# Kernel tuning notes

Measured on AMD Instinct MI355X. Metric: run time of the kernel, lower is better.

## Reference

```python
import jax, jax.numpy as jnp
import numpy as np

N_HEADS = 16
D_K = 64
DIM = 1024
NEG = -1e12
LN_EPS = 1e-5


def setup_inputs() -> dict:
    key = jax.random.key(0)
    ks = jax.random.split(key, 8)
    B, S, D = 2, 2048, DIM
    H, K = N_HEADS, D_K
    f = lambda k, shp: jax.random.normal(k, shp, dtype=jnp.float32)
    scale = 0.02
    return {
        "input_Q": f(ks[0], (B, S, D)),
        "input_K": f(ks[1], (B, S, D)),
        "input_V": f(ks[2], (B, S, D)),
        "attention_mask": jax.random.randint(ks[3], (B, S), 0, 2, dtype=jnp.int32),
        "W_Q": f(ks[4], (H * K, D)) * scale,  # nn.Linear weight layout [out, in]
        "W_K": f(ks[5], (H * K, D)) * scale,
        "W_V": f(ks[6], (H * K, D)) * scale,
        "W_O": f(ks[7], (D, H * K)) * scale,
        "gamma": jnp.ones((D,), jnp.float32),
        "beta": jnp.zeros((D,), jnp.float32),
    }


def reference(input_Q, input_K, input_V, attention_mask, W_Q, W_K, W_V, W_O, gamma, beta):
    B, S, D = input_Q.shape

    def proj(x, W):  # [B,S,D] @ [HK,D]^T -> [B,H,S,K]
        return (x @ W.T).reshape(B, S, N_HEADS, D_K).transpose(0, 2, 1, 3)

    Q = proj(input_Q, W_Q)
    K = proj(input_K, W_K)
    V = proj(input_V, W_V)

    scores = jnp.einsum('bhqk,bhsk->bhqs', Q, K) / np.float32(np.sqrt(D_K))

    # Faithful reproduction of scores_mask (including its inverted-looking logic):
    # mask = clamp(padding_mask + strict_upper_tri - 1, min=0); scores += (1-mask)*NEG
    am = attention_mask.astype(scores.dtype)[:, None, None, :]          # [B,1,1,S]
    low_tri = jnp.triu(jnp.ones((S, S), scores.dtype), k=1)             # 1 - tril(ones)
    m = jnp.maximum(am + low_tri - 1.0, 0.0)
    scores = scores + (1.0 - m) * NEG

    attn = jax.nn.softmax(scores, axis=-1)
    ctx = jnp.einsum('bhqs,bhsk->bhqk', attn, V)                        # [B,H,S,K]
    ctx = ctx.transpose(0, 2, 1, 3).reshape(B, S, N_HEADS * D_K)

    out = ctx @ W_O.T + input_Q                                         # fc + residual
    mu = jnp.mean(out, axis=-1, keepdims=True)
    var = jnp.var(out, axis=-1, keepdims=True)
    return (out - mu) / jnp.sqrt(var + LN_EPS) * gamma + beta
```

## Files before the change

kernel.cpp:

```cpp
#include <hip/hip_runtime.h>

#define NH    16
#define DK    64
#define DIM   1024
#define BATCH 2
#define SEQ   2048
#define MROWS (BATCH*SEQ)
#define BK    64
#define QSCALE 0.18033688011112043f
#define SENT   -44.0f
#define PCONST 5.684341886080802e-14f

typedef unsigned short bfraw;
typedef __attribute__((ext_vector_type(8))) __bf16 bf16x8;
typedef __attribute__((ext_vector_type(8))) unsigned short u16x8;
typedef __attribute__((ext_vector_type(4))) float f32x4;

__device__ __forceinline__ float bf2f(bfraw u) {
    union { unsigned int i; float f; } x; x.i = ((unsigned int)u) << 16; return x.f;
}
__device__ __forceinline__ bfraw f2bf(float f) {
    union { float f; unsigned int i; } x; x.f = f;
    unsigned int r = x.i + 0x7FFFu + ((x.i >> 16) & 1u);
    return (bfraw)(r >> 16);
}
__device__ __forceinline__ bfraw f2bf_trunc(float f) {
    union { float f; unsigned int i; } x; x.f = f;
    return (bfraw)(x.i >> 16);
}
__device__ __forceinline__ float fexp2(float x) {
#if __has_builtin(__builtin_amdgcn_exp2f)
    return __builtin_amdgcn_exp2f(x);
#else
    return exp2f(x);
#endif
}

__device__ __forceinline__ void gload16(const bfraw* g, bfraw* l) {
#if __has_builtin(__builtin_amdgcn_global_load_lds)
    __builtin_amdgcn_global_load_lds(
        (const __attribute__((address_space(1))) unsigned int*)g,
        (__attribute__((address_space(3))) unsigned int*)l, 16, 0, 0);
#else
    *(u16x8*)(l + (threadIdx.x & 63) * 8) = *(const u16x8*)g;
#endif
}

__device__ __forceinline__ float block_reduce(float val, float* rbuf, int op) {
    const int lane = threadIdx.x & 63, wave = threadIdx.x >> 6;
    #pragma unroll
    for (int off = 32; off; off >>= 1) {
        float o = __shfl_xor(val, off, 64);
        val = op ? (val + o) : fmaxf(val, o);
    }
    if (lane == 0) rbuf[wave] = val;
    __syncthreads();
    float r = op ? (rbuf[0] + rbuf[1] + rbuf[2] + rbuf[3])
                 : fmaxf(fmaxf(rbuf[0], rbuf[1]), fmaxf(rbuf[2], rbuf[3]));
    __syncthreads();
    return r;
}

__global__ __launch_bounds__(256) void cvt_kernel(
        const float* __restrict__ x0, const float* __restrict__ x1, const float* __restrict__ x2,
        const float* __restrict__ w0, const float* __restrict__ w1, const float* __restrict__ w2,
        const float* __restrict__ w3, bfraw* __restrict__ Xb, bfraw* __restrict__ Wb) {
    const int t = blockIdx.y;
    const float* src; bfraw* dst; int n;
    if (t < 3) { src = (t == 0) ? x0 : (t == 1) ? x1 : x2; dst = Xb + t * (MROWS * DIM); n = MROWS * DIM; }
    else { int u = t - 3; src = (u == 0) ? w0 : (u == 1) ? w1 : (u == 2) ? w2 : w3;
           dst = Wb + u * (DIM * DIM); n = DIM * DIM; }
    int idx = (blockIdx.x * 256 + threadIdx.x) * 8;
    if (idx >= n) return;
    f32x4 a = *(const f32x4*)(src + idx);
    f32x4 b = *(const f32x4*)(src + idx + 4);
    u16x8 o;
    #pragma unroll
    for (int j = 0; j < 4; j++) { o[j] = f2bf(a[j]); o[4 + j] = f2bf(b[j]); }
    *(u16x8*)(dst + idx) = o;
}

__device__ __forceinline__ void gemm128(const bfraw* __restrict__ A, const bfraw* __restrict__ B,
                                        int m0, int n0, f32x4 acc[4][4]) {
    __shared__ __align__(16) bfraw As[128 * BK];
    __shared__ __align__(16) bfraw Bs[128 * BK];
    const int tid = threadIdx.x, wave = tid >> 6;
    const int lane = tid & 63, lrow = lane & 15, quad = lane >> 4;
    const int wy = wave >> 1, wx = wave & 1;
    const int swz = lrow & 7;
    const int srow = tid >> 3;
    const int schunk = ((tid & 7) ^ (srow & 7)) << 3;
    const bfraw* ga[4]; const bfraw* gb[4];
    #pragma unroll
    for (int g = 0; g < 4; g++) {
        ga[g] = A + (m0 + g * 32 + srow) * DIM + schunk;
        gb[g] = B + (n0 + g * 32 + srow) * DIM + schunk;
    }
    bfraw* la = As + wave * 512;
    bfraw* lb = Bs + wave * 512;

    #pragma unroll
    for (int i = 0; i < 4; i++)
        #pragma unroll
        for (int j = 0; j < 4; j++) { f32x4 z = {0.f, 0.f, 0.f, 0.f}; acc[i][j] = z; }

    for (int k0 = 0; k0 < DIM; k0 += BK) {
        __syncthreads();
        #pragma unroll
        for (int g = 0; g < 4; g++) gload16(ga[g] + k0, la + g * 2048);
        #pragma unroll
        for (int g = 0; g < 4; g++) gload16(gb[g] + k0, lb + g * 2048);
        __syncthreads();
        #pragma unroll
        for (int ks = 0; ks < 2; ks++) {
            const int c = (ks << 2) | quad;
            bf16x8 af[4], bfg[4];
            #pragma unroll
            for (int mi = 0; mi < 4; mi++)
                af[mi] = *(const bf16x8*)&As[(wy * 64 + mi * 16 + lrow) * BK + ((c ^ swz) << 3)];
            #pragma unroll
            for (int ni = 0; ni < 4; ni++)
                bfg[ni] = *(const bf16x8*)&Bs[(wx * 64 + ni * 16 + lrow) * BK + ((c ^ swz) << 3)];
            #pragma unroll
            for (int mi = 0; mi < 4; mi++)
                #pragma unroll
                for (int ni = 0; ni < 4; ni++)
                    acc[mi][ni] = __builtin_amdgcn_mfma_f32_16x16x32_bf16(af[mi], bfg[ni], acc[mi][ni], 0, 0, 0);
        }
    }
}

__global__ __launch_bounds__(256) void qkv_gemm(
        const bfraw* __restrict__ Xb, const bfraw* __restrict__ Wb,
        bfraw* __restrict__ Qp, bfraw* __restrict__ Kp, bfraw* __restrict__ Vt) {
    const int which = blockIdx.z;
    const bfraw* A = Xb + which * (MROWS * DIM);
    const bfraw* B = Wb + which * (DIM * DIM);
    bfraw* O = (which == 0) ? Qp : (which == 1) ? Kp : Vt;
    const int m0 = blockIdx.x * 128, n0 = blockIdx.y * 128;
    f32x4 acc[4][4];
    gemm128(A, B, m0, n0, acc);
    const int lane = threadIdx.x & 63, wave = threadIdx.x >> 6;
    const int lrow = lane & 15, quad = lane >> 4;
    const int wy = wave >> 1, wx = wave & 1;
    const float scale = (which == 0) ? QSCALE : 1.0f;
    #pragma unroll
    for (int mi = 0; mi < 4; mi++)
        #pragma unroll
        for (int ni = 0; ni < 4; ni++)
            #pragma unroll
            for (int i = 0; i < 4; i++) {
                int m = m0 + wy * 64 + mi * 16 + quad * 4 + i;
                int n = n0 + wx * 64 + ni * 16 + lrow;
                int b = m >> 11, s = m & (SEQ - 1), h = n >> 6, kk = n & (DK - 1);
                bfraw v = f2bf(acc[mi][ni][i] * scale);
                if (which == 2) O[(((b * NH + h) * DK) + kk) * SEQ + s] = v;
                else            O[(((b * NH + h) * SEQ) + s) * DK + kk] = v;
            }
}

__global__ __launch_bounds__(256) void vsum_kernel(const bfraw* __restrict__ Vt,
                                                   float* __restrict__ Scum) {
    __shared__ float Ts[32][65];
    const int bh = blockIdx.x, tid = threadIdx.x;
    const int d = tid & 63, part = tid >> 6;
    const bfraw* vrow = Vt + (bh * DK + d) * SEQ;
    for (int qt = part * 8; qt < part * 8 + 8; qt++) {
        float s = 0.f;
        #pragma unroll
        for (int j = 0; j < 64; j += 8) {
            u16x8 v = *(const u16x8*)(vrow + qt * 64 + j);
            #pragma unroll
            for (int e = 0; e < 8; e++) s += bf2f(v[e]);
        }
        Ts[qt][d] = s;
    }
    __syncthreads();
    if (tid < 64) {
        float run = 0.f;
        for (int qt = 0; qt < 32; qt++) {
            Scum[(bh * 32 + qt) * 64 + tid] = run;
            run += Ts[qt][tid];
        }
    }
}

__global__ __launch_bounds__(256) void attn_flash(
        const bfraw* __restrict__ Qp, const bfraw* __restrict__ Kp, const bfraw* __restrict__ Vt,
        const float* __restrict__ Scum, const int* __restrict__ mask, bfraw* __restrict__ Ctx) {
    __shared__ __align__(16) bfraw Ks[64 * 72];
    __shared__ __align__(16) bfraw Vs[64 * 72];
    __shared__ __align__(16) bfraw Pw[4][16 * 68];
    __shared__ unsigned short Mk[SEQ];
    const int bh = blockIdx.x, qt = blockIdx.y;
    const int b = bh >> 4, h = bh & 15;
    const int tid = threadIdx.x, wave = tid >> 6, lane = tid & 63;
    const int lrow = lane & 15, quad = lane >> 4;
    const int baseK = ((b * NH + h) * SEQ) * DK;
    const int baseV = ((b * NH + h) * DK) * SEQ;
    const int qbase = qt * 64 + wave * 16;
    const int ldr = tid >> 2, ldc = (tid & 3) << 4;
    const int diagKt = qt * 64;

    for (int i = tid; i < SEQ; i += 256) Mk[i] = (unsigned short)(mask[b * SEQ + i] != 0);

    bf16x8 qf[2];
    qf[0] = *(const bf16x8*)(Qp + baseK + (qbase + lrow) * DK + quad * 8);
    qf[1] = *(const bf16x8*)(Qp + baseK + (qbase + lrow) * DK + 32 + quad * 8);

    f32x4 O[4]; float lsum[4];
    #pragma unroll
    for (int n = 0; n < 4; n++) {
        float base = PCONST * Scum[(bh * 32 + qt) * 64 + n * 16 + lrow];
        #pragma unroll
        for (int i = 0; i < 4; i++) O[n][i] = base;
    }
    #pragma unroll
    for (int i = 0; i < 4; i++) lsum[i] = 0.f;

    __syncthreads();

    for (int kt0 = diagKt; kt0 < SEQ; kt0 += 64) {
        u16x8 k0 = *(const u16x8*)(Kp + baseK + (kt0 + ldr) * DK + ldc);
        u16x8 k1 = *(const u16x8*)(Kp + baseK + (kt0 + ldr) * DK + ldc + 8);
        u16x8 v0 = *(const u16x8*)(Vt + baseV + ldr * SEQ + kt0 + ldc);
        u16x8 v1 = *(const u16x8*)(Vt + baseV + ldr * SEQ + kt0 + ldc + 8);
        __syncthreads();
        *(u16x8*)&Ks[ldr * 72 + ldc]     = k0;
        *(u16x8*)&Ks[ldr * 72 + ldc + 8] = k1;
        *(u16x8*)&Vs[ldr * 72 + ldc]     = v0;
        *(u16x8*)&Vs[ldr * 72 + ldc + 8] = v1;
        __syncthreads();

        f32x4 S[4];
        #pragma unroll
        for (int n = 0; n < 4; n++) {
            f32x4 z = {0.f, 0.f, 0.f, 0.f}; S[n] = z;
            #pragma unroll
            for (int ks = 0; ks < 2; ks++) {
                bf16x8 kb = *(const bf16x8*)&Ks[(n * 16 + lrow) * 72 + ks * 32 + quad * 8];
                S[n] = __builtin_amdgcn_mfma_f32_16x16x32_bf16(qf[ks], kb, S[n], 0, 0, 0);
            }
        }

        float p[4][4];
        if (kt0 == diagKt) {
            #pragma unroll
            for (int n = 0; n < 4; n++) {
                int s = kt0 + n * 16 + lrow;
                bool mk = (Mk[s] != 0);
                #pragma unroll
                for (int i = 0; i < 4; i++) {
                    bool valid = mk && (s > qbase + quad * 4 + i);
                    p[n][i] = fexp2(valid ? S[n][i] : SENT);
                }
            }
        } else {
            #pragma unroll
            for (int n = 0; n < 4; n++) {
                bool mk = (Mk[kt0 + n * 16 + lrow] != 0);
                #pragma unroll
                for (int i = 0; i < 4; i++) p[n][i] = fexp2(mk ? S[n][i] : SENT);
            }
        }

        #pragma unroll
        for (int i = 0; i < 4; i++) lsum[i] += (p[0][i] + p[1][i]) + (p[2][i] + p[3][i]);

        #pragma unroll
        for (int n = 0; n < 4; n++)
            #pragma unroll
            for (int i = 0; i < 4; i++)
                Pw[wave][(quad * 4 + i) * 68 + n * 16 + lrow] = f2bf_trunc(p[n][i]);

        bf16x8 pa0 = *(const bf16x8*)&Pw[wave][lrow * 68 + quad * 8];
        bf16x8 pa1 = *(const bf16x8*)&Pw[wave][lrow * 68 + 32 + quad * 8];
        #pragma unroll
        for (int n = 0; n < 4; n++)
            #pragma unroll
            for (int ks = 0; ks < 2; ks++) {
                bf16x8 vb = *(const bf16x8*)&Vs[(n * 16 + lrow) * 72 + ks * 32 + quad * 8];
                O[n] = __builtin_amdgcn_mfma_f32_16x16x32_bf16(ks ? pa1 : pa0, vb, O[n], 0, 0, 0);
            }
    }

    float inv[4];
    #pragma unroll
    for (int i = 0; i < 4; i++) {
        float r = lsum[i];
        #pragma unroll
        for (int off = 1; off < 16; off <<= 1) r += __shfl_xor(r, off, 64);
        inv[i] = 1.0f / (r + (float)diagKt * PCONST);
    }
    #pragma unroll
    for (int n = 0; n < 4; n++)
        #pragma unroll
        for (int i = 0; i < 4; i++)
            Ctx[(b * SEQ + qbase + quad * 4 + i) * DIM + h * DK + n * 16 + lrow] = f2bf(O[n][i] * inv[i]);
}

__global__ __launch_bounds__(256) void out_gemm(
        const bfraw* __restrict__ Ctx, const bfraw* __restrict__ WoB, float* __restrict__ C) {
    const int m0 = blockIdx.x * 128, n0 = blockIdx.y * 128;
    f32x4 acc[4][4];
    gemm128(Ctx, WoB, m0, n0, acc);
    const int lane = threadIdx.x & 63, wave = threadIdx.x >> 6;
    const int lrow = lane & 15, quad = lane >> 4;
    const int wy = wave >> 1, wx = wave & 1;
    #pragma unroll
    for (int mi = 0; mi < 4; mi++)
        #pragma unroll
        for (int ni = 0; ni < 4; ni++)
            #pragma unroll
            for (int i = 0; i < 4; i++) {
                int m = m0 + wy * 64 + mi * 16 + quad * 4 + i;
                int n = n0 + wx * 64 + ni * 16 + lrow;
                C[m * DIM + n] = acc[mi][ni][i];
            }
}

__global__ __launch_bounds__(256) void ln_kernel(
        const float* __restrict__ C, const float* __restrict__ Xq,
        const float* __restrict__ gamma, const float* __restrict__ beta,
        float* __restrict__ out) {
    __shared__ float rbuf[4];
    const int m = blockIdx.x, tid = threadIdx.x;
    const float* crow = C + m * DIM;
    const float* xrow = Xq + m * DIM;
    float v[4]; float s = 0.f, s2 = 0.f;
    #pragma unroll
    for (int i = 0; i < 4; i++) {
        int d = tid + (i << 8);
        float x = crow[d] + xrow[d];
        v[i] = x; s += x; s2 += x * x;
    }
    float S  = block_reduce(s,  rbuf, 1);
    float S2 = block_reduce(s2, rbuf, 1);
    float mu  = S * (1.0f / DIM);
    float var = S2 * (1.0f / DIM) - mu * mu;
    float rstd = rsqrtf(var + 1e-5f);
    #pragma unroll
    for (int i = 0; i < 4; i++) {
        int d = tid + (i << 8);
        out[m * DIM + d] = (v[i] - mu) * rstd * gamma[d] + beta[d];
    }
}

extern "C" void kernel_launch(void* const* d_in, const int* in_sizes, int n_in,
                              void* d_out, int out_size, void* d_ws, size_t ws_size,
                              hipStream_t stream) {
    const float* Xq    = (const float*)d_in[0];
    const float* Xk    = (const float*)d_in[1];
    const float* Xv    = (const float*)d_in[2];
    const int*   mask  = (const int*)  d_in[3];
    const float* Wq    = (const float*)d_in[4];
    const float* Wk    = (const float*)d_in[5];
    const float* Wv    = (const float*)d_in[6];
    const float* Wo    = (const float*)d_in[7];
    const float* gamma = (const float*)d_in[8];
    const float* beta  = (const float*)d_in[9];
    float* out = (float*)d_out;

    char* ws = (char*)d_ws;
    bfraw* Xb   = (bfraw*)(ws);
    bfraw* Wb   = (bfraw*)(ws + (24u << 20));
    bfraw* Qp   = (bfraw*)(ws + (32u << 20));
    bfraw* Kp   = (bfraw*)(ws + (40u << 20));
    bfraw* Vt   = (bfraw*)(ws + (48u << 20));
    bfraw* Ctx  = (bfraw*)(ws + (56u << 20));
    float* C    = (float*)(ws);
    float* Scum = (float*)(ws + (16u << 20));

    dim3 blk(256);
    cvt_kernel<<<dim3(MROWS * DIM / (256 * 8), 7), blk, 0, stream>>>(Xq, Xk, Xv, Wq, Wk, Wv, Wo, Xb, Wb);
    qkv_gemm  <<<dim3(MROWS / 128, DIM / 128, 3),  blk, 0, stream>>>(Xb, Wb, Qp, Kp, Vt);
    vsum_kernel<<<dim3(BATCH * NH),                blk, 0, stream>>>(Vt, Scum);
    attn_flash<<<dim3(BATCH * NH, SEQ / 64),       blk, 0, stream>>>(Qp, Kp, Vt, Scum, mask, Ctx);
    out_gemm  <<<dim3(MROWS / 128, DIM / 128),     blk, 0, stream>>>(Ctx, Wb + 3 * (DIM * DIM), C);
    ln_kernel <<<dim3(MROWS),                      blk, 0, stream>>>(C, Xq, gamma, beta, out);
}
```

Before: 243.3 us.

## Widen attention query tile to 128 rows with swizzled direct-to-LDS K/V loads

Result: slower. 264.3 us (+8.6%).

```diff
diff --git a/kernel.cpp b/kernel.cpp
--- a/kernel.cpp
+++ b/kernel.cpp
@@ -188,115 +188,135 @@
 __global__ __launch_bounds__(256) void attn_flash(
         const bfraw* __restrict__ Qp, const bfraw* __restrict__ Kp, const bfraw* __restrict__ Vt,
         const float* __restrict__ Scum, const int* __restrict__ mask, bfraw* __restrict__ Ctx) {
-    __shared__ __align__(16) bfraw Ks[64 * 72];
-    __shared__ __align__(16) bfraw Vs[64 * 72];
-    __shared__ __align__(16) bfraw Pw[4][16 * 68];
+    __shared__ __align__(16) bfraw Ks[64 * 64];
+    __shared__ __align__(16) bfraw Vs[64 * 64];
+    __shared__ __align__(16) bfraw Pw[4][32 * 68];
     __shared__ unsigned short Mk[SEQ];
-    const int bh = blockIdx.x, qt = blockIdx.y;
+    const int bh = blockIdx.x, yy = blockIdx.y;
+    const int qt = (yy & 1) ? (15 - (yy >> 1)) : (yy >> 1);
     const int b = bh >> 4, h = bh & 15;
     const int tid = threadIdx.x, wave = tid >> 6, lane = tid & 63;
     const int lrow = lane & 15, quad = lane >> 4;
     const int baseK = ((b * NH + h) * SEQ) * DK;
     const int baseV = ((b * NH + h) * DK) * SEQ;
-    const int qbase = qt * 64 + wave * 16;
-    const int ldr = tid >> 2, ldc = (tid & 3) << 4;
-    const int diagKt = qt * 64;
+    const int blockDiag = qt * 128;
+    const int qbase = blockDiag + wave * 32;
+    const int tW = qt * 2 + (wave >> 1);
+    const int wstart = blockDiag + (wave >> 1) * 64;
+    const int srow8 = lane >> 3;
+    const int gchunk = ((lane & 7) ^ srow8) << 3;
 
     for (int i = tid; i < SEQ; i += 256) Mk[i] = (unsigned short)(mask[b * SEQ + i] != 0);
 
-    bf16x8 qf[2];
-    qf[0] = *(const bf16x8*)(Qp + baseK + (qbase + lrow) * DK + quad * 8);
-    qf[1] = *(const bf16x8*)(Qp + baseK + (qbase + lrow) * DK + 32 + quad * 8);
-
-    f32x4 O[4]; float lsum[4];
+    bf16x8 qf[2][2];
+    #pragma unroll
+    for (int set = 0; set < 2; set++)
+        #pragma unroll
+        for (int ks = 0; ks < 2; ks++)
+            qf[set][ks] = *(const bf16x8*)(Qp + baseK + (qbase + set * 16 + lrow) * DK + ks * 32 + quad * 8);
+
+    f32x4 Oa[2][4]; float lsum[2][4];
     #pragma unroll
     for (int n = 0; n < 4; n++) {
-        float base = PCONST * Scum[(bh * 32 + qt) * 64 + n * 16 + lrow];
-        #pragma unroll
-        for (int i = 0; i < 4; i++) O[n][i] = base;
-    }
-    #pragma unroll
-    for (int i = 0; i < 4; i++) lsum[i] = 0.f;
-
-    __syncthreads();
-
-    for (int kt0 = diagKt; kt0 < SEQ; kt0 += 64) {
-        u16x8 k0 = *(const u16x8*)(Kp + baseK + (kt0 + ldr) * DK + ldc);
-        u16x8 k1 = *(const u16x8*)(Kp + baseK + (kt0 + ldr) * DK + ldc + 8);
-        u16x8 v0 = *(const u16x8*)(Vt + baseV + ldr * SEQ + kt0 + ldc);
-        u16x8 v1 = *(const u16x8*)(Vt + baseV + ldr * SEQ + kt0 + ldc + 8);
+        float base = PCONST * Scum[(bh * 32 + tW) * 64 + n * 16 + lrow];
+        #pragma unroll
+        for (int set = 0; set < 2; set++) {
+            #pragma unroll
+            for (int i = 0; i < 4; i++) Oa[set][n][i] = base;
+        }
+    }
+    #pragma unroll
+    for (int set = 0; set < 2; set++)
+        #pragma unroll
+        for (int i = 0; i < 4; i++) lsum[set][i] = 0.f;
+
+    for (int kt0 = blockDiag; kt0 < SEQ; kt0 += 64) {
         __syncthreads();
-        *(u16x8*)&Ks[ldr * 72 + ldc]     = k0;
-        *(u16x8*)&Ks[ldr * 72 + ldc + 8] = k1;
-        *(u16x8*)&Vs[ldr * 72 + ldc]     = v0;
-        *(u16x8*)&Vs[ldr * 72 + ldc + 8] = v1;
+        #pragma unroll
+        for (int r = 0; r < 2; r++) {
+            const int row0 = r * 32 + wave * 8;
+            gload16(Kp + baseK + (kt0 + row0 + srow8) * DK + gchunk, Ks + row0 * 64);
+            gload16(Vt + baseV + (row0 + srow8) * SEQ + kt0 + gchunk, Vs + row0 * 64);
+        }
         __syncthreads();
 
-        f32x4 S[4];
-        #pragma unroll
-        for (int n = 0; n < 4; n++) {
-            f32x4 z = {0.f, 0.f, 0.f, 0.f}; S[n] = z;
-            #pragma unroll
-            for (int ks = 0; ks < 2; ks++) {
-                bf16x8 kb = *(const bf16x8*)&Ks[(n * 16 + lrow) * 72 + ks * 32 + quad * 8];
-                S[n] = __builtin_amdgcn_mfma_f32_16x16x32_bf16(qf[ks], kb, S[n], 0, 0, 0);
+        if (kt0 >= wstart) {
+            bf16x8 kf[2][4];
+            #pragma unroll
+            for (int n = 0; n < 4; n++) {
+                const int s = n * 16 + lrow;
+                #pragma unroll
+                for (int ks = 0; ks < 2; ks++)
+                    kf[ks][n] = *(const bf16x8*)&Ks[s * 64 + ((((ks << 2) | quad) ^ (s & 7)) << 3)];
             }
-        }
-
-        float p[4][4];
-        if (kt0 == diagKt) {
-            #pragma unroll
-            for (int n = 0; n < 4; n++) {
-                int s = kt0 + n * 16 + lrow;
-                bool mk = (Mk[s] != 0);
-                #pragma unroll
-                for (int i = 0; i < 4; i++) {
-                    bool valid = mk && (s > qbase + quad * 4 + i);
-                    p[n][i] = fexp2(valid ? S[n][i] : SENT);
+            f32x4 S[2][4];
+            #pragma unroll
+            for (int set = 0; set < 2; set++)
+                #pragma unroll
+                for (int n = 0; n < 4; n++) {
+                    f32x4 z = {0.f, 0.f, 0.f, 0.f};
+                    z = __builtin_amdgcn_mfma_f32_16x16x32_bf16(qf[set][0], kf[0][n], z, 0, 0, 0);
+                    S[set][n] = __builtin_amdgcn_mfma_f32_16x16x32_bf16(qf[set][1], kf[1][n], S[set][n] = z, 0, 0, 0);
+                }
+
+            const bool diagzone = (kt0 < blockDiag + 128);
+            #pragma unroll
+            for (int set = 0; set < 2; set++) {
+                #pragma unroll
+                for (int n = 0; n < 4; n++) {
+                    const int s = kt0 + n * 16 + lrow;
+                    const bool mk = (Mk[s] != 0);
+                    #pragma unroll
+                    for (int i = 0; i < 4; i++) {
+                        bool valid = diagzone ? (mk && (s > qbase + set * 16 + quad * 4 + i)) : mk;
+                        float p = fexp2(valid ? S[set][n][i] : SENT);
+                        lsum[set][i] += p;
+                        Pw[wave][(set * 16 + quad * 4 + i) * 68 + n * 16 + lrow] = f2bf_trunc(p);
+                    }
                 }
             }
-        } else {
+
+            bf16x8 vf[2][4];
             #pragma unroll
             for (int n = 0; n < 4; n++) {
-                bool mk = (Mk[kt0 + n * 16 + lrow] != 0);
-                #pragma unroll
-                for (int i = 0; i < 4; i++) p[n][i] = fexp2(mk ? S[n][i] : SENT);
+                const int d = n * 16 + lrow;
+                #pragma unroll
+                for (int ks = 0; ks < 2; ks++)
+                    vf[ks][n] = *(const bf16x8*)&Vs[d * 64 + ((((ks << 2) | quad) ^ (d & 7)) << 3)];
             }
-        }
-
-        #pragma unroll
-        for (int i = 0; i < 4; i++) lsum[i] += (p[0][i] + p[1][i]) + (p[2][i] + p[3][i]);
-
+            bf16x8 pf[2][2];
+            #pragma unroll
+            for (int set = 0; set < 2; set++)
+                #pragma unroll
+                for (int ks = 0; ks < 2; ks++)
+                    pf[set][ks] = *(const bf16x8*)&Pw[wave][(set * 16 + lrow) * 68 + ks * 32 + quad * 8];
+            #pragma unroll
+            for (int set = 0; set < 2; set++)
+                #pragma unroll
+                for (int n = 0; n < 4; n++) {
+                    Oa[set][n] = __builtin_amdgcn_mfma_f32_16x16x32_bf16(pf[set][0], vf[0][n], Oa[set][n], 0, 0, 0);
+                    Oa[set][n] = __builtin_amdgcn_mfma_f32_16x16x32_bf16(pf[set][1], vf[1][n], Oa[set][n], 0, 0, 0);
+                }
+        }
+    }
+
+    #pragma unroll
+    for (int set = 0; set < 2; set++) {
+        float inv[4];
+        #pragma unroll
+        for (int i = 0; i < 4; i++) {
+            float r = lsum[set][i];
+            #pragma unroll
+            for (int off = 1; off < 16; off <<= 1) r += __shfl_xor(r, off, 64);
+            inv[i] = 1.0f / (r + (float)(tW * 64) * PCONST);
+        }
         #pragma unroll
         for (int n = 0; n < 4; n++)
             #pragma unroll
             for (int i = 0; i < 4; i++)
-                Pw[wave][(quad * 4 + i) * 68 + n * 16 + lrow] = f2bf_trunc(p[n][i]);
-
-        bf16x8 pa0 = *(const bf16x8*)&Pw[wave][lrow * 68 + quad * 8];
-        bf16x8 pa1 = *(const bf16x8*)&Pw[wave][lrow * 68 + 32 + quad * 8];
-        #pragma unroll
-        for (int n = 0; n < 4; n++)
-            #pragma unroll
-            for (int ks = 0; ks < 2; ks++) {
-                bf16x8 vb = *(const bf16x8*)&Vs[(n * 16 + lrow) * 72 + ks * 32 + quad * 8];
-                O[n] = __builtin_amdgcn_mfma_f32_16x16x32_bf16(ks ? pa1 : pa0, vb, O[n], 0, 0, 0);
-            }
-    }
-
-    float inv[4];
-    #pragma unroll
-    for (int i = 0; i < 4; i++) {
-        float r = lsum[i];
-        #pragma unroll
-        for (int off = 1; off < 16; off <<= 1) r += __shfl_xor(r, off, 64);
-        inv[i] = 1.0f / (r + (float)diagKt * PCONST);
-    }
-    #pragma unroll
-    for (int n = 0; n < 4; n++)
-        #pragma unroll
-        for (int i = 0; i < 4; i++)
-            Ctx[(b * SEQ + qbase + quad * 4 + i) * DIM + h * DK + n * 16 + lrow] = f2bf(O[n][i] * inv[i]);
+                Ctx[(b * SEQ + qbase + set * 16 + quad * 4 + i) * DIM + h * DK + n * 16 + lrow]
+                    = f2bf(Oa[set][n][i] * inv[i]);
+    }
 }
 
 __global__ __launch_bounds__(256) void out_gemm(
@@ -375,7 +395,7 @@
     cvt_kernel<<<dim3(MROWS * DIM / (256 * 8), 7), blk, 0, stream>>>(Xq, Xk, Xv, Wq, Wk, Wv, Wo, Xb, Wb);
     qkv_gemm  <<<dim3(MROWS / 128, DIM / 128, 3),  blk, 0, stream>>>(Xb, Wb, Qp, Kp, Vt);
     vsum_kernel<<<dim3(BATCH * NH),                blk, 0, stream>>>(Vt, Scum);
-    attn_flash<<<dim3(BATCH * NH, SEQ / 64),       blk, 0, stream>>>(Qp, Kp, Vt, Scum, mask, Ctx);
+    attn_flash<<<dim3(BATCH * NH, SEQ / 128),      blk, 0, stream>>>(Qp, Kp, Vt, Scum, mask, Ctx);
     out_gemm  <<<dim3(MROWS / 128, DIM / 128),     blk, 0, stream>>>(Ctx, Wb + 3 * (DIM * DIM), C);
     ln_kernel <<<dim3(MROWS),                      blk, 0, stream>>>(C, Xq, gamma, beta, out);
 }
```

## Swizzle K/V shared tiles with XOR layout and reorder query tiles for balance

Applied to the files above, without the earlier changes.

New measurement: 236.0 us. 1.03x faster.

```diff
diff --git a/kernel.cpp b/kernel.cpp
--- a/kernel.cpp
+++ b/kernel.cpp
@@ -188,19 +188,25 @@
 __global__ __launch_bounds__(256) void attn_flash(
         const bfraw* __restrict__ Qp, const bfraw* __restrict__ Kp, const bfraw* __restrict__ Vt,
         const float* __restrict__ Scum, const int* __restrict__ mask, bfraw* __restrict__ Ctx) {
-    __shared__ __align__(16) bfraw Ks[64 * 72];
-    __shared__ __align__(16) bfraw Vs[64 * 72];
+    __shared__ __align__(16) bfraw Ks[64 * 64];
+    __shared__ __align__(16) bfraw Vs[64 * 64];
     __shared__ __align__(16) bfraw Pw[4][16 * 68];
     __shared__ unsigned short Mk[SEQ];
-    const int bh = blockIdx.x, qt = blockIdx.y;
+    const int bh = blockIdx.x, yy = blockIdx.y;
+    const int gg = yy >> 3, jj = yy & 7;
+    const int qt = (gg == 0) ? jj : (gg == 1) ? (31 - jj) : (gg == 2) ? (8 + jj) : (23 - jj);
     const int b = bh >> 4, h = bh & 15;
     const int tid = threadIdx.x, wave = tid >> 6, lane = tid & 63;
     const int lrow = lane & 15, quad = lane >> 4;
     const int baseK = ((b * NH + h) * SEQ) * DK;
     const int baseV = ((b * NH + h) * DK) * SEQ;
     const int qbase = qt * 64 + wave * 16;
-    const int ldr = tid >> 2, ldc = (tid & 3) << 4;
     const int diagKt = qt * 64;
+    const int ldr = tid >> 2;
+    const int cg0 = (tid & 3) << 1;
+    const int ldc = cg0 << 3;
+    const int e7 = ldr & 7;
+    const int cl0 = ((cg0 ^ e7) << 3), cl1 = (((cg0 | 1) ^ e7) << 3);
 
     for (int i = tid; i < SEQ; i += 256) Mk[i] = (unsigned short)(mask[b * SEQ + i] != 0);
 
@@ -226,21 +232,23 @@
         u16x8 v0 = *(const u16x8*)(Vt + baseV + ldr * SEQ + kt0 + ldc);
         u16x8 v1 = *(const u16x8*)(Vt + baseV + ldr * SEQ + kt0 + ldc + 8);
         __syncthreads();
-        *(u16x8*)&Ks[ldr * 72 + ldc]     = k0;
-        *(u16x8*)&Ks[ldr * 72 + ldc + 8] = k1;
-        *(u16x8*)&Vs[ldr * 72 + ldc]     = v0;
-        *(u16x8*)&Vs[ldr * 72 + ldc + 8] = v1;
+        *(u16x8*)&Ks[ldr * 64 + cl0] = k0;
+        *(u16x8*)&Ks[ldr * 64 + cl1] = k1;
+        *(u16x8*)&Vs[ldr * 64 + cl0] = v0;
+        *(u16x8*)&Vs[ldr * 64 + cl1] = v1;
         __syncthreads();
 
         f32x4 S[4];
         #pragma unroll
         for (int n = 0; n < 4; n++) {
-            f32x4 z = {0.f, 0.f, 0.f, 0.f}; S[n] = z;
+            const int s = n * 16 + lrow;
+            f32x4 z = {0.f, 0.f, 0.f, 0.f};
             #pragma unroll
             for (int ks = 0; ks < 2; ks++) {
-                bf16x8 kb = *(const bf16x8*)&Ks[(n * 16 + lrow) * 72 + ks * 32 + quad * 8];
-                S[n] = __builtin_amdgcn_mfma_f32_16x16x32_bf16(qf[ks], kb, S[n], 0, 0, 0);
-            }
+                bf16x8 kb = *(const bf16x8*)&Ks[s * 64 + ((((ks << 2) | quad) ^ (s & 7)) << 3)];
+                z = __builtin_amdgcn_mfma_f32_16x16x32_bf16(qf[ks], kb, z, 0, 0, 0);
+            }
+            S[n] = z;
         }
 
         float p[4][4];
@@ -276,12 +284,14 @@
         bf16x8 pa0 = *(const bf16x8*)&Pw[wave][lrow * 68 + quad * 8];
         bf16x8 pa1 = *(const bf16x8*)&Pw[wave][lrow * 68 + 32 + quad * 8];
         #pragma unroll
-        for (int n = 0; n < 4; n++)
+        for (int n = 0; n < 4; n++) {
+            const int d = n * 16 + lrow;
             #pragma unroll
             for (int ks = 0; ks < 2; ks++) {
-                bf16x8 vb = *(const bf16x8*)&Vs[(n * 16 + lrow) * 72 + ks * 32 + quad * 8];
+                bf16x8 vb = *(const bf16x8*)&Vs[d * 64 + ((((ks << 2) | quad) ^ (d & 7)) << 3)];
                 O[n] = __builtin_amdgcn_mfma_f32_16x16x32_bf16(ks ? pa1 : pa0, vb, O[n], 0, 0, 0);
             }
+        }
     }
 
     float inv[4];
```
